# Performance work log

Hardware: AMD Instinct MI355X
Metric: run time of the kernel (lower is better)

Reference implementation:

```python
import jax, jax.numpy as jnp
import numpy as np

FEATURE_DIM = 768
NUM_HEADS = 16
HEAD_DIM = FEATURE_DIM // NUM_HEADS
SCALE = HEAD_DIM ** -0.5


def setup_inputs() -> dict:
    key = jax.random.key(0)
    ks = jax.random.split(key, 9)
    B, N, C = 4, 2048, FEATURE_DIM
    s = 0.02
    return {
        "x": jax.random.normal(ks[0], (B, N, C), dtype=jnp.float32),
        "wq": jax.random.normal(ks[1], (C, C), dtype=jnp.float32) * s,
        "bq": jax.random.normal(ks[2], (C,), dtype=jnp.float32) * s,
        "wk": jax.random.normal(ks[3], (C, C), dtype=jnp.float32) * s,
        "bk": jax.random.normal(ks[4], (C,), dtype=jnp.float32) * s,
        "wv": jax.random.normal(ks[5], (C, C), dtype=jnp.float32) * s,
        "bv": jax.random.normal(ks[6], (C,), dtype=jnp.float32) * s,
        "wo": jax.random.normal(ks[7], (C, C), dtype=jnp.float32) * s,
        "bo": jax.random.normal(ks[8], (C,), dtype=jnp.float32) * s,
    }


def reference(x, wq, bq, wk, bk, wv, bv, wo, bo):
    B, N, C = x.shape
    H, D = NUM_HEADS, HEAD_DIM
    # Linear layers use weight of shape (out, in): y = x @ W.T + b
    def proj(w, b):
        return (jnp.einsum("bnc,dc->bnd", x, w) + b).reshape(B, N, H, D).transpose(0, 2, 1, 3)
    q = proj(wq, bq)  # [B,H,N,D]
    k = proj(wk, bk)
    v = proj(wv, bv)
    attn = jnp.einsum("bhnd,bhmd->bhnm", q, k) * SCALE
    attn = jax.nn.softmax(attn, axis=-1)  # dropout = identity (eval mode)
    y = jnp.einsum("bhnm,bhmd->bhnd", attn, v).transpose(0, 2, 1, 3).reshape(B, N, C)
    y = y + x
    out = jnp.einsum("bnc,dc->bnd", y, wo) + bo
    out = out + y
    return out + x
```

## Files before the change

kernel.cpp:

```cpp
#include <hip/hip_runtime.h>
#include <hip/hip_bf16.h>

#define B_ 4
#define N_ 2048
#define C_ 768
#define H_ 16
#define D_ 48
#define SCALE_ 0.14433756729740643f
#define LOG2E_ 1.44269504088896f

using bf16 = __hip_bfloat16;
using bf16x8 = __attribute__((ext_vector_type(8))) short;
using f32x4  = __attribute__((ext_vector_type(4))) float;
using f32x16 = __attribute__((ext_vector_type(16))) float;
using u32x2  = __attribute__((ext_vector_type(2))) unsigned int;
using u32x4  = __attribute__((ext_vector_type(4))) unsigned int;

__device__ __forceinline__ unsigned short f2b(float f) {
  bf16 h = __float2bfloat16(f);
  return *reinterpret_cast<unsigned short*>(&h);
}
__device__ __forceinline__ unsigned int pack2(float lo, float hi) {
  return (unsigned int)f2b(lo) | ((unsigned int)f2b(hi) << 16);
}
__device__ __forceinline__ unsigned int pk2(float lo, float hi) {
  unsigned int r;
  asm("v_cvt_pk_bf16_f32 %0, %1, %2" : "=v"(r) : "v"(lo), "v"(hi));
  return r;
}
__device__ __forceinline__ uint4 ld8f_cvt(const float* p) {
  float4 a = *reinterpret_cast<const float4*>(p);
  float4 b = *reinterpret_cast<const float4*>(p + 4);
  uint4 u;
  u.x = pack2(a.x, a.y); u.y = pack2(a.z, a.w);
  u.z = pack2(b.x, b.y); u.w = pack2(b.z, b.w);
  return u;
}
__device__ __forceinline__ void gload_lds16(const bf16* g, bf16* l) {
  __builtin_amdgcn_global_load_lds(
      (const __attribute__((address_space(1))) unsigned int*)g,
      (__attribute__((address_space(3))) unsigned int*)l, 16, 0, 0);
}

__global__ __launch_bounds__(256) void cvt_bf16(
    const float* __restrict__ x,  const float* __restrict__ wq,
    const float* __restrict__ wk, const float* __restrict__ wv,
    const float* __restrict__ wo,
    bf16* __restrict__ xb, bf16* __restrict__ wqkvb, bf16* __restrict__ wob,
    bf16* __restrict__ vfp)
{
  const int job = blockIdx.y;
  if (job == 5) {
    for (int u = blockIdx.x * 256 + threadIdx.x; u < 64 * 128 * 32;
         u += gridDim.x * 256) {
      const int m5i = u & 15, hb = (u >> 4) & 1, n4 = (u >> 5) & 127,
                bh = u >> 12;
      const short fill = (m5i == 0) ? (short)0x3F80 : (short)0;
      const bf16x8 o = {fill, fill, fill, fill, fill, fill, fill, fill};
      *(bf16x8*)(vfp + (size_t)bh * 131072 + n4 * 1024 + 512 + hb * 256 +
                 (16 + m5i) * 8) = o;
    }
    return;
  }
  const float* src; bf16* dst; int n;
  if (job == 0)      { src = x;  dst = xb;              n = B_ * N_ * C_; }
  else if (job == 1) { src = wq; dst = wqkvb;           n = C_ * C_; }
  else if (job == 2) { src = wk; dst = wqkvb + C_ * C_; n = C_ * C_; }
  else if (job == 3) { src = wv; dst = wqkvb + 2 * C_ * C_; n = C_ * C_; }
  else               { src = wo; dst = wob;             n = C_ * C_; }
  const int stride = gridDim.x * 256 * 8;
  for (int i = (blockIdx.x * 256 + threadIdx.x) * 8; i < n; i += stride)
    *(uint4*)(dst + i) = ld8f_cvt(src + i);
}

__global__ __launch_bounds__(256) void gemm_qkv(
    const bf16* __restrict__ A, const bf16* __restrict__ Bw,
    const float* __restrict__ bq, const float* __restrict__ bk,
    const float* __restrict__ bv,
    bf16* __restrict__ Q, bf16* __restrict__ K, bf16* __restrict__ Vf)
{
  __shared__ __align__(16) bf16 As[128 * 64];
  __shared__ __align__(16) bf16 Bs[128 * 64];

  const int tid  = threadIdx.x;
  const int lane = tid & 63, wid = tid >> 6;
  const int wm = (wid >> 1) * 64, wn = (wid & 1) * 64;
  const int row0 = blockIdx.y * 128, col0 = blockIdx.x * 128;
  const int mb = lane & 15, g4 = lane >> 4;
  const int srow = lane >> 3;
  const int schunk = (lane & 7) ^ (srow & 7);

  f32x4 acc[4][4];
#pragma unroll
  for (int i = 0; i < 4; ++i)
#pragma unroll
    for (int j = 0; j < 4; ++j) acc[i][j] = (f32x4){0.f, 0.f, 0.f, 0.f};

  for (int k0 = 0; k0 < C_; k0 += 64) {
#pragma unroll
    for (int t = 0; t < 4; ++t) {
      const int rt = wid * 32 + t * 8;
      gload_lds16(A  + (size_t)(row0 + rt + srow) * C_ + k0 + schunk * 8,
                  As + rt * 64);
      gload_lds16(Bw + (size_t)(col0 + rt + srow) * C_ + k0 + schunk * 8,
                  Bs + rt * 64);
    }
    __syncthreads();
#pragma unroll
    for (int ks = 0; ks < 2; ++ks) {
      const int kchunk = ks * 4 + g4;
      bf16x8 af[4], bfr[4];
#pragma unroll
      for (int i = 0; i < 4; ++i) {
        const int row = wm + i * 16 + mb;
        af[i] = *(const bf16x8*)(As + row * 64 + (kchunk ^ (row & 7)) * 8);
      }
#pragma unroll
      for (int j = 0; j < 4; ++j) {
        const int col = wn + j * 16 + mb;
        bfr[j] = *(const bf16x8*)(Bs + col * 64 + (kchunk ^ (col & 7)) * 8);
      }
#pragma unroll
      for (int i = 0; i < 4; ++i)
#pragma unroll
        for (int j = 0; j < 4; ++j)
          acc[i][j] = __builtin_amdgcn_mfma_f32_16x16x32_bf16(af[i], bfr[j], acc[i][j], 0, 0, 0);
    }
    __syncthreads();
  }

  const int z = blockIdx.x / 6;
  const int b_ = row0 >> 11;
  const int nb = (row0 & (N_ - 1)) + wm;
  if (z < 2) {
    const float* bias = (z == 0) ? bq : bk;
    bf16* dst = (z == 0) ? Q : K;
    const float sc = (z == 0) ? (SCALE_ * LOG2E_) : 1.0f;
#pragma unroll
    for (int j = 0; j < 4; ++j) {
      const int oo = col0 - z * 768 + wn + j * 16 + mb;
      const int h = oo / D_, d = oo % D_;
      const float bb = bias[oo];
      bf16* slabp = dst + (size_t)(b_ * H_ + h) * (N_ * D_);
      const int dpart = (d >> 4) * 512 + ((d >> 3) & 1) * 256 + (d & 7);
#pragma unroll
      for (int i = 0; i < 4; ++i) {
        const int base2 = ((nb >> 5) + (i >> 1)) * 1536 + dpart;
        const int mlo = (i & 1) * 16 + g4 * 4;
#pragma unroll
        for (int reg = 0; reg < 4; ++reg)
          slabp[base2 + (mlo + reg) * 8] =
              __float2bfloat16((acc[i][j][reg] + bb) * sc);
      }
    }
  } else {
#pragma unroll
    for (int j = 0; j < 4; ++j) {
      const int oo = col0 - 2 * 768 + wn + j * 16 + mb;
      const int h = oo / D_, d = oo % D_;
      const float bb = bv[oo];
      bf16* slabp = Vf + (size_t)(b_ * H_ + h) * (N_ * 64);
      const int dpart = (d >> 5) * 512 + ((g4 >> 1) * 32 + (d & 31)) * 8 +
                        (g4 & 1) * 4;
#pragma unroll
      for (int i = 0; i < 4; ++i) {
        u32x2 wv;
        wv.x = pk2(acc[i][j][0] + bb, acc[i][j][1] + bb);
        wv.y = pk2(acc[i][j][2] + bb, acc[i][j][3] + bb);
        *(u32x2*)(slabp + ((nb >> 4) + i) * 1024 + dpart) = wv;
      }
    }
  }
}

__global__ __launch_bounds__(256, 4) void attn_mfma(
    const bf16* __restrict__ Qf, const bf16* __restrict__ Kf,
    const bf16* __restrict__ Vf, const float* __restrict__ x,
    bf16* __restrict__ Yb)
{
  __shared__ __align__(16) bf16 Ls[2 * 7168];

  const int tid  = threadIdx.x;
  const int lane = tid & 63, wid = tid >> 6;
  const int m5 = lane & 31, hi = lane >> 5;
  const int bh = blockIdx.x;
  const int b_ = bh >> 4, h = bh & 15;
  const int q0 = blockIdx.y * 128 + wid * 32;
  const size_t slab  = (size_t)bh * (N_ * D_);
  const size_t slabV = (size_t)bh * (N_ * 64);

  bf16x8 qf[3];
  const int kgq = q0 >> 5;
#pragma unroll
  for (int kc = 0; kc < 3; ++kc)
    qf[kc] = *(const bf16x8*)(Qf + slab + (size_t)(((kgq * 3 + kc) * 64) + lane) * 8);

  f32x16 zf;
#pragma unroll
  for (int r = 0; r < 16; ++r) zf[r] = 0.f;

  f32x16 Oacc[2];
#pragma unroll
  for (int dt = 0; dt < 2; ++dt)
#pragma unroll
    for (int r = 0; r < 16; ++r) Oacc[dt][r] = 0.f;

  const bf16* kb = Kf + slab  + (size_t)lane * 8;
  const bf16* vb = Vf + slabV + (size_t)lane * 8;
  auto stage = [&](int t, int buf) {
    bf16* dstb = Ls + buf * 7168;
    const bf16* kt = kb + (size_t)t * 3072;
    const bf16* vt = vb + (size_t)t * 4096;
    for (int c = wid; c < 14; c += 4) {
      if (c < 6) gload_lds16(kt + c * 512, dstb + c * 512);
      else       gload_lds16(vt + (c - 6) * 512, dstb + c * 512);
    }
  };

  auto sub = [&](int buf, int s) {
    const bf16* Lb = Ls + buf * 7168 + (size_t)lane * 8;
    bf16x8 kf[3], vA[2][2];
#pragma unroll
    for (int kc = 0; kc < 3; ++kc)
      kf[kc] = *(const bf16x8*)(Lb + (s * 3 + kc) * 512);
#pragma unroll
    for (int ks = 0; ks < 2; ++ks)
#pragma unroll
      for (int dt = 0; dt < 2; ++dt)
        vA[ks][dt] = *(const bf16x8*)(Lb + (6 + s * 4 + ks * 2 + dt) * 512);
    f32x16 S;
    S = __builtin_amdgcn_mfma_f32_32x32x16_bf16(kf[0], qf[0], zf, 0, 0, 0);
    S = __builtin_amdgcn_mfma_f32_32x32x16_bf16(kf[1], qf[1], S, 0, 0, 0);
    S = __builtin_amdgcn_mfma_f32_32x32x16_bf16(kf[2], qf[2], S, 0, 0, 0);
#pragma unroll
    for (int r = 0; r < 16; ++r)
      S[r] = __builtin_amdgcn_exp2f(S[r]);
#pragma unroll
    for (int ks = 0; ks < 2; ++ks) {
      const int qa = ks * 2;
      const unsigned A0 = pk2(S[4 * qa + 0], S[4 * qa + 1]);
      const unsigned A1 = pk2(S[4 * qa + 2], S[4 * qa + 3]);
      const unsigned B0 = pk2(S[4 * qa + 4], S[4 * qa + 5]);
      const unsigned B1 = pk2(S[4 * qa + 6], S[4 * qa + 7]);
      const u32x2 r02 = __builtin_amdgcn_permlane32_swap(A0, B0, false, false);
      const u32x2 r13 = __builtin_amdgcn_permlane32_swap(A1, B1, false, false);
      u32x4 pw;
      pw.x = r02.x; pw.y = r13.x; pw.z = r02.y; pw.w = r13.y;
      const bf16x8 pb = (bf16x8)pw;
      Oacc[0] = __builtin_amdgcn_mfma_f32_32x32x16_bf16(vA[ks][0], pb, Oacc[0], 0, 0, 0);
      Oacc[1] = __builtin_amdgcn_mfma_f32_32x32x16_bf16(vA[ks][1], pb, Oacc[1], 0, 0, 0);
    }
  };

  stage(0, 0);
  __syncthreads();
  int buf = 0;
#pragma unroll 1
  for (int t = 0; t < 32; ++t) {
    if (t + 1 < 32) stage(t + 1, buf ^ 1);
    sub(buf, 0);
    sub(buf, 1);
    __syncthreads();
    buf ^= 1;
  }

  const float lf = Oacc[1][8];
  const unsigned lu = __builtin_bit_cast(unsigned, lf);
  const u32x2 lsw = __builtin_amdgcn_permlane32_swap(lu, lu, false, false);
  const float Lv = __builtin_bit_cast(float, lsw.x);
  const float inv = 1.f / Lv;

  const int n = q0 + m5;
  const size_t rowoff = ((size_t)(b_ * N_ + n)) * C_ + h * D_;
#pragma unroll
  for (int qq = 0; qq < 4; ++qq) {
    const size_t off = rowoff + 8 * qq + 4 * hi;
    const float4 xr = *(const float4*)(x + off);
    u32x2 wv;
    wv.x = pk2(Oacc[0][4 * qq + 0] * inv + xr.x, Oacc[0][4 * qq + 1] * inv + xr.y);
    wv.y = pk2(Oacc[0][4 * qq + 2] * inv + xr.z, Oacc[0][4 * qq + 3] * inv + xr.w);
    *(u32x2*)(Yb + off) = wv;
  }
#pragma unroll
  for (int qq = 0; qq < 2; ++qq) {
    const size_t off = rowoff + 32 + 8 * qq + 4 * hi;
    const float4 xr = *(const float4*)(x + off);
    u32x2 wv;
    wv.x = pk2(Oacc[1][4 * qq + 0] * inv + xr.x, Oacc[1][4 * qq + 1] * inv + xr.y);
    wv.y = pk2(Oacc[1][4 * qq + 2] * inv + xr.z, Oacc[1][4 * qq + 3] * inv + xr.w);
    *(u32x2*)(Yb + off) = wv;
  }
}

__global__ __launch_bounds__(256) void gemm_out(
    const bf16* __restrict__ Yb, const bf16* __restrict__ Bw,
    const float* __restrict__ bo, const float* __restrict__ x,
    float* __restrict__ out)
{
  __shared__ __align__(16) bf16 As[128 * 64];
  __shared__ __align__(16) bf16 Bs[128 * 64];

  const int tid  = threadIdx.x;
  const int lane = tid & 63, wid = tid >> 6;
  const int wm = (wid >> 1) * 64, wn = (wid & 1) * 64;
  const int row0 = blockIdx.y * 128, col0 = blockIdx.x * 128;
  const int mb = lane & 15, g4 = lane >> 4;
  const int srow = lane >> 3;
  const int schunk = (lane & 7) ^ (srow & 7);

  f32x4 acc[4][4];
#pragma unroll
  for (int i = 0; i < 4; ++i)
#pragma unroll
    for (int j = 0; j < 4; ++j) acc[i][j] = (f32x4){0.f, 0.f, 0.f, 0.f};

  for (int k0 = 0; k0 < C_; k0 += 64) {
#pragma unroll
    for (int t = 0; t < 4; ++t) {
      const int rt = wid * 32 + t * 8;
      gload_lds16(Yb + (size_t)(row0 + rt + srow) * C_ + k0 + schunk * 8,
                  As + rt * 64);
      gload_lds16(Bw + (size_t)(col0 + rt + srow) * C_ + k0 + schunk * 8,
                  Bs + rt * 64);
    }
    __syncthreads();
#pragma unroll
    for (int ks = 0; ks < 2; ++ks) {
      const int kchunk = ks * 4 + g4;
      bf16x8 af[4], bfr[4];
#pragma unroll
      for (int i = 0; i < 4; ++i) {
        const int row = wm + i * 16 + mb;
        af[i] = *(const bf16x8*)(As + row * 64 + (kchunk ^ (row & 7)) * 8);
      }
#pragma unroll
      for (int j = 0; j < 4; ++j) {
        const int col = wn + j * 16 + mb;
        bfr[j] = *(const bf16x8*)(Bs + col * 64 + (kchunk ^ (col & 7)) * 8);
      }
#pragma unroll
      for (int i = 0; i < 4; ++i)
#pragma unroll
        for (int j = 0; j < 4; ++j)
          acc[i][j] = __builtin_amdgcn_mfma_f32_16x16x32_bf16(af[i], bfr[j], acc[i][j], 0, 0, 0);
    }
    __syncthreads();
  }

  const int crow = g4 * 4;
#pragma unroll
  for (int j = 0; j < 4; ++j) {
    const int o = col0 + wn + j * 16 + mb;
    const float bb = bo[o];
#pragma unroll
    for (int i = 0; i < 4; ++i) {
#pragma unroll
      for (int reg = 0; reg < 4; ++reg) {
        const int r = row0 + wm + i * 16 + crow + reg;
        const size_t off = (size_t)r * C_ + o;
        out[off] = acc[i][j][reg] + bb + __bfloat162float(Yb[off]) + x[off];
      }
    }
  }
}

extern "C" void kernel_launch(void* const* d_in, const int* in_sizes, int n_in,
                              void* d_out, int out_size, void* d_ws, size_t ws_size,
                              hipStream_t stream)
{
  const float* x  = (const float*)d_in[0];
  const float* wq = (const float*)d_in[1];
  const float* bq = (const float*)d_in[2];
  const float* wk = (const float*)d_in[3];
  const float* bk = (const float*)d_in[4];
  const float* wv = (const float*)d_in[5];
  const float* bv = (const float*)d_in[6];
  const float* wo = (const float*)d_in[7];
  const float* bo = (const float*)d_in[8];
  float* out = (float*)d_out;

  const size_t nEl  = (size_t)B_ * N_ * C_;
  const size_t wEl  = (size_t)C_ * C_;
  const size_t vfEl = (size_t)B_ * H_ * N_ * 64;
  bf16* Q     = (bf16*)d_ws;
  bf16* K     = Q + nEl;
  bf16* Vf    = K + nEl;
  bf16* Yb    = Vf + vfEl;
  bf16* xb    = Yb + nEl;
  bf16* wqkvb = xb + nEl;
  bf16* wob   = wqkvb + 3 * wEl;

  dim3 gcvt(768, 6);
  cvt_bf16<<<gcvt, dim3(256), 0, stream>>>(x, wq, wk, wv, wo, xb, wqkvb, wob, Vf);

  dim3 gqkv(18, 64);
  gemm_qkv<<<gqkv, dim3(256), 0, stream>>>(xb, wqkvb, bq, bk, bv, Q, K, Vf);

  dim3 gattn(B_ * H_, N_ / 128);
  attn_mfma<<<gattn, dim3(256), 0, stream>>>(Q, K, Vf, x, Yb);

  dim3 gout(6, 64);
  gemm_out<<<gout, dim3(256), 0, stream>>>(Yb, wob, bo, x, out);
}
```

Baseline: 250.6 us.

## Process two 32-query tiles per wave in attention to reuse K/V fragments

Each attention wave now handles 64 query rows, as two 32-row tiles, instead of 32. The K and V fragments read from LDS are reused across both tiles. The block covers 256 queries, so the grid halves and occupancy bounds drop to 2 blocks per SM. This halves LDS reads and global K/V staging per query, at the cost of doubled accumulator registers and fewer blocks (512) available to fill the GPU.

```diff
diff --git a/kernel.cpp b/kernel.cpp
--- a/kernel.cpp
+++ b/kernel.cpp
@@ -173,7 +173,7 @@
   }
 }
 
-__global__ __launch_bounds__(256, 4) void attn_mfma(
+__global__ __launch_bounds__(256, 2) void attn_mfma(
     const bf16* __restrict__ Qf, const bf16* __restrict__ Kf,
     const bf16* __restrict__ Vf, const float* __restrict__ x,
     bf16* __restrict__ Yb)
@@ -185,25 +185,27 @@
   const int m5 = lane & 31, hi = lane >> 5;
   const int bh = blockIdx.x;
   const int b_ = bh >> 4, h = bh & 15;
-  const int q0 = blockIdx.y * 128 + wid * 32;
+  const int q0 = blockIdx.y * 256 + wid * 64;
   const size_t slab  = (size_t)bh * (N_ * D_);
   const size_t slabV = (size_t)bh * (N_ * 64);
 
-  bf16x8 qf[3];
+  bf16x8 qfA[3], qfB[3];
   const int kgq = q0 >> 5;
 #pragma unroll
-  for (int kc = 0; kc < 3; ++kc)
-    qf[kc] = *(const bf16x8*)(Qf + slab + (size_t)(((kgq * 3 + kc) * 64) + lane) * 8);
+  for (int kc = 0; kc < 3; ++kc) {
+    qfA[kc] = *(const bf16x8*)(Qf + slab + (size_t)(((kgq * 3 + kc) * 64) + lane) * 8);
+    qfB[kc] = *(const bf16x8*)(Qf + slab + (size_t)((((kgq + 1) * 3 + kc) * 64) + lane) * 8);
+  }
 
   f32x16 zf;
 #pragma unroll
   for (int r = 0; r < 16; ++r) zf[r] = 0.f;
 
-  f32x16 Oacc[2];
+  f32x16 OA[2], OB[2];
 #pragma unroll
   for (int dt = 0; dt < 2; ++dt)
 #pragma unroll
-    for (int r = 0; r < 16; ++r) Oacc[dt][r] = 0.f;
+    for (int r = 0; r < 16; ++r) { OA[dt][r] = 0.f; OB[dt][r] = 0.f; }
 
   const bf16* kb = Kf + slab  + (size_t)lane * 8;
   const bf16* vb = Vf + slabV + (size_t)lane * 8;
@@ -217,21 +219,7 @@
     }
   };
 
-  auto sub = [&](int buf, int s) {
-    const bf16* Lb = Ls + buf * 7168 + (size_t)lane * 8;
-    bf16x8 kf[3], vA[2][2];
-#pragma unroll
-    for (int kc = 0; kc < 3; ++kc)
-      kf[kc] = *(const bf16x8*)(Lb + (s * 3 + kc) * 512);
-#pragma unroll
-    for (int ks = 0; ks < 2; ++ks)
-#pragma unroll
-      for (int dt = 0; dt < 2; ++dt)
-        vA[ks][dt] = *(const bf16x8*)(Lb + (6 + s * 4 + ks * 2 + dt) * 512);
-    f32x16 S;
-    S = __builtin_amdgcn_mfma_f32_32x32x16_bf16(kf[0], qf[0], zf, 0, 0, 0);
-    S = __builtin_amdgcn_mfma_f32_32x32x16_bf16(kf[1], qf[1], S, 0, 0, 0);
-    S = __builtin_amdgcn_mfma_f32_32x32x16_bf16(kf[2], qf[2], S, 0, 0, 0);
+  auto smpv = [&](f32x16& S, f32x16& O0, f32x16& O1, bf16x8 (&vA)[2][2]) {
 #pragma unroll
     for (int r = 0; r < 16; ++r)
       S[r] = __builtin_amdgcn_exp2f(S[r]);
@@ -247,8 +235,35 @@
       u32x4 pw;
       pw.x = r02.x; pw.y = r13.x; pw.z = r02.y; pw.w = r13.y;
       const bf16x8 pb = (bf16x8)pw;
-      Oacc[0] = __builtin_amdgcn_mfma_f32_32x32x16_bf16(vA[ks][0], pb, Oacc[0], 0, 0, 0);
-      Oacc[1] = __builtin_amdgcn_mfma_f32_32x32x16_bf16(vA[ks][1], pb, Oacc[1], 0, 0, 0);
+      O0 = __builtin_amdgcn_mfma_f32_32x32x16_bf16(vA[ks][0], pb, O0, 0, 0, 0);
+      O1 = __builtin_amdgcn_mfma_f32_32x32x16_bf16(vA[ks][1], pb, O1, 0, 0, 0);
+    }
+  };
+
+  auto sub = [&](int buf, int s) {
+    const bf16* Lb = Ls + buf * 7168 + (size_t)lane * 8;
+    bf16x8 kf[3], vA[2][2];
+#pragma unroll
+    for (int kc = 0; kc < 3; ++kc)
+      kf[kc] = *(const bf16x8*)(Lb + (s * 3 + kc) * 512);
+#pragma unroll
+    for (int ks = 0; ks < 2; ++ks)
+#pragma unroll
+      for (int dt = 0; dt < 2; ++dt)
+        vA[ks][dt] = *(const bf16x8*)(Lb + (6 + s * 4 + ks * 2 + dt) * 512);
+    {
+      f32x16 S;
+      S = __builtin_amdgcn_mfma_f32_32x32x16_bf16(kf[0], qfA[0], zf, 0, 0, 0);
+      S = __builtin_amdgcn_mfma_f32_32x32x16_bf16(kf[1], qfA[1], S, 0, 0, 0);
+      S = __builtin_amdgcn_mfma_f32_32x32x16_bf16(kf[2], qfA[2], S, 0, 0, 0);
+      smpv(S, OA[0], OA[1], vA);
+    }
+    {
+      f32x16 S;
+      S = __builtin_amdgcn_mfma_f32_32x32x16_bf16(kf[0], qfB[0], zf, 0, 0, 0);
+      S = __builtin_amdgcn_mfma_f32_32x32x16_bf16(kf[1], qfB[1], S, 0, 0, 0);
+      S = __builtin_amdgcn_mfma_f32_32x32x16_bf16(kf[2], qfB[2], S, 0, 0, 0);
+      smpv(S, OB[0], OB[1], vA);
     }
   };
 
@@ -264,32 +279,35 @@
     buf ^= 1;
   }
 
-  const float lf = Oacc[1][8];
-  const unsigned lu = __builtin_bit_cast(unsigned, lf);
-  const u32x2 lsw = __builtin_amdgcn_permlane32_swap(lu, lu, false, false);
-  const float Lv = __builtin_bit_cast(float, lsw.x);
-  const float inv = 1.f / Lv;
-
-  const int n = q0 + m5;
-  const size_t rowoff = ((size_t)(b_ * N_ + n)) * C_ + h * D_;
-#pragma unroll
-  for (int qq = 0; qq < 4; ++qq) {
-    const size_t off = rowoff + 8 * qq + 4 * hi;
-    const float4 xr = *(const float4*)(x + off);
-    u32x2 wv;
-    wv.x = pk2(Oacc[0][4 * qq + 0] * inv + xr.x, Oacc[0][4 * qq + 1] * inv + xr.y);
-    wv.y = pk2(Oacc[0][4 * qq + 2] * inv + xr.z, Oacc[0][4 * qq + 3] * inv + xr.w);
-    *(u32x2*)(Yb + off) = wv;
-  }
-#pragma unroll
-  for (int qq = 0; qq < 2; ++qq) {
-    const size_t off = rowoff + 32 + 8 * qq + 4 * hi;
-    const float4 xr = *(const float4*)(x + off);
-    u32x2 wv;
-    wv.x = pk2(Oacc[1][4 * qq + 0] * inv + xr.x, Oacc[1][4 * qq + 1] * inv + xr.y);
-    wv.y = pk2(Oacc[1][4 * qq + 2] * inv + xr.z, Oacc[1][4 * qq + 3] * inv + xr.w);
-    *(u32x2*)(Yb + off) = wv;
-  }
+  auto epi = [&](const f32x16& O0, const f32x16& O1, int qbase) {
+    const float lf = O1[8];
+    const unsigned lu = __builtin_bit_cast(unsigned, lf);
+    const u32x2 lsw = __builtin_amdgcn_permlane32_swap(lu, lu, false, false);
+    const float Lv = __builtin_bit_cast(float, lsw.x);
+    const float inv = 1.f / Lv;
+    const int n = qbase + m5;
+    const size_t rowoff = ((size_t)(b_ * N_ + n)) * C_ + h * D_;
+#pragma unroll
+    for (int qq = 0; qq < 4; ++qq) {
+      const size_t off = rowoff + 8 * qq + 4 * hi;
+      const float4 xr = *(const float4*)(x + off);
+      u32x2 wv;
+      wv.x = pk2(O0[4 * qq + 0] * inv + xr.x, O0[4 * qq + 1] * inv + xr.y);
+      wv.y = pk2(O0[4 * qq + 2] * inv + xr.z, O0[4 * qq + 3] * inv + xr.w);
+      *(u32x2*)(Yb + off) = wv;
+    }
+#pragma unroll
+    for (int qq = 0; qq < 2; ++qq) {
+      const size_t off = rowoff + 32 + 8 * qq + 4 * hi;
+      const float4 xr = *(const float4*)(x + off);
+      u32x2 wv;
+      wv.x = pk2(O1[4 * qq + 0] * inv + xr.x, O1[4 * qq + 1] * inv + xr.y);
+      wv.y = pk2(O1[4 * qq + 2] * inv + xr.z, O1[4 * qq + 3] * inv + xr.w);
+      *(u32x2*)(Yb + off) = wv;
+    }
+  };
+  epi(OA[0], OA[1], q0);
+  epi(OB[0], OB[1], q0 + 32);
 }
 
 __global__ __launch_bounds__(256) void gemm_out(
@@ -396,7 +414,7 @@
   dim3 gqkv(18, 64);
   gemm_qkv<<<gqkv, dim3(256), 0, stream>>>(xb, wqkvb, bq, bk, bv, Q, K, Vf);
 
-  dim3 gattn(B_ * H_, N_ / 128);
+  dim3 gattn(B_ * H_, N_ / 256);
   attn_mfma<<<gattn, dim3(256), 0, stream>>>(Q, K, Vf, x, Yb);
 
   dim3 gout(6, 64);
```

After: 243.5 us. -2.8%, faster.
